# Kernel tuning notes

Hardware: AMD Instinct MI355X
Metric: run time of the kernel (lower is better)

## Reference

```python
import jax, jax.numpy as jnp
import numpy as np

EPS = 1e-12
B, S, H, NH = 4, 2048, 512, 8
DH = H // NH

def layernorm(x, g, b):
    mu = jnp.mean(x, axis=-1, keepdims=True)
    var = jnp.mean((x - mu) ** 2, axis=-1, keepdims=True)
    return (x - mu) * jax.lax.rsqrt(var + EPS) * g + b

def setup_inputs() -> dict:
    key = jax.random.key(0)
    ks = jax.random.split(key, 12)
    s = 0.02
    return {
        "hidden_states": jax.random.normal(ks[0], (B, S, H), dtype=jnp.float32),
        "attention_mask": jnp.zeros((B, 1, 1, S), dtype=jnp.float32),
        "ln1_g": jnp.ones((H,), jnp.float32), "ln1_b": jnp.zeros((H,), jnp.float32),
        "wq": jax.random.normal(ks[1], (H, H), jnp.float32) * s, "bq": jnp.zeros((H,), jnp.float32),
        "wk": jax.random.normal(ks[2], (H, H), jnp.float32) * s, "bk": jnp.zeros((H,), jnp.float32),
        "wv": jax.random.normal(ks[3], (H, H), jnp.float32) * s, "bv": jnp.zeros((H,), jnp.float32),
        "wo": jax.random.normal(ks[4], (H, H), jnp.float32) * s, "bo": jnp.zeros((H,), jnp.float32),
        "ln2_g": jnp.ones((H,), jnp.float32), "ln2_b": jnp.zeros((H,), jnp.float32),
    }

def _heads(x):  # [B,S,H] -> [B,NH,S,DH]
    return x.reshape(B, S, NH, DH).transpose(0, 2, 1, 3)

def reference(hidden_states, attention_mask, ln1_g, ln1_b, wq, bq, wk, bk, wv, bv, wo, bo, ln2_g, ln2_b):
    h = layernorm(hidden_states, ln1_g, ln1_b)  # Pre-LN
    q = _heads(h @ wq.T + bq)
    k = _heads(h @ wk.T + bk)
    v = _heads(h @ wv.T + bv)
    scores = jnp.einsum("bhqd,bhkd->bhqk", q, k) / jnp.sqrt(jnp.float32(DH))
    scores = scores + attention_mask  # additive BERT mask
    probs = jax.nn.softmax(scores, axis=-1)
    ctx = jnp.einsum("bhqk,bhkd->bhqd", probs, v)
    ctx = ctx.transpose(0, 2, 1, 3).reshape(B, S, H)
    # BertSelfOutput: LN(dense(ctx) + residual), residual is the LN'd hidden per module code
    out = layernorm(ctx @ wo.T + bo + h, ln2_g, ln2_b)
    return out
```

## Files before the change

### kernel.cpp

```cpp
#include <hip/hip_runtime.h>

typedef __bf16 bf16;
typedef __bf16 bf16x2 __attribute__((ext_vector_type(2)));
typedef __bf16 bf16x4 __attribute__((ext_vector_type(4)));
typedef __bf16 bf16x8 __attribute__((ext_vector_type(8)));
typedef float f32x4 __attribute__((ext_vector_type(4)));

typedef __attribute__((address_space(1))) const void g_void;
typedef __attribute__((address_space(3))) void l_void;

constexpr int Bsz = 4, S = 2048, H = 512, NH = 8, DH = 64;
constexpr int M = Bsz * S;
constexpr int K = H;
constexpr int WELEM = H * H;
constexpr float LOG2E  = 1.44269504f;
constexpr float QSCALE = 0.125f * LOG2E;

__global__ __launch_bounds__(256) void convert_w(
    const float* __restrict__ w0, const float* __restrict__ w1,
    const float* __restrict__ w2, const float* __restrict__ w3,
    bf16* __restrict__ dst) {
    int y = blockIdx.y;
    const float* src = (y == 0) ? w0 : (y == 1) ? w1 : (y == 2) ? w2 : w3;
    bf16* d = dst + (size_t)y * WELEM;
    int i = (blockIdx.x * 256 + threadIdx.x) * 4;
    float4 v = *(const float4*)(src + i);
    bf16x4 o;
    o.x = (bf16)v.x; o.y = (bf16)v.y; o.z = (bf16)v.z; o.w = (bf16)v.w;
    *(bf16x4*)(d + i) = o;
}

__global__ __launch_bounds__(256) void scale_mask(
    const float* __restrict__ m, float* __restrict__ out) {
    int i = blockIdx.x * 256 + threadIdx.x;
    out[i] = m[i] * LOG2E;
}

__global__ __launch_bounds__(256) void ln_f32_bf16(
    const float* __restrict__ x, const float* __restrict__ g,
    const float* __restrict__ b, bf16* __restrict__ y) {
    int row = blockIdx.x;
    int t = threadIdx.x;
    float2 xv = *(const float2*)(x + (size_t)row * H + t * 2);
    float v0 = xv.x, v1 = xv.y;
    float s = v0 + v1, s2 = v0 * v0 + v1 * v1;
    for (int off = 1; off < 64; off <<= 1) {
        s  += __shfl_xor(s,  off, 64);
        s2 += __shfl_xor(s2, off, 64);
    }
    __shared__ float red[8];
    int wid = t >> 6;
    if ((t & 63) == 0) { red[wid * 2] = s; red[wid * 2 + 1] = s2; }
    __syncthreads();
    s  = red[0] + red[2] + red[4] + red[6];
    s2 = red[1] + red[3] + red[5] + red[7];
    float mu  = s * (1.0f / H);
    float var = s2 * (1.0f / H) - mu * mu;
    float inv = rsqrtf(var + 1e-12f);
    float2 gv = *(const float2*)(g + t * 2);
    float2 bv = *(const float2*)(b + t * 2);
    bf16x2 out;
    out.x = (bf16)((v0 - mu) * inv * gv.x + bv.x);
    out.y = (bf16)((v1 - mu) * inv * gv.y + bv.y);
    *(bf16x2*)(y + (size_t)row * H + t * 2) = out;
}

__global__ __launch_bounds__(256) void ln_bf16_f32(
    const bf16* __restrict__ x, const float* __restrict__ g,
    const float* __restrict__ b, float* __restrict__ y) {
    int row = blockIdx.x;
    int t = threadIdx.x;
    bf16x2 xv = *(const bf16x2*)(x + (size_t)row * H + t * 2);
    float v0 = (float)xv.x, v1 = (float)xv.y;
    float s = v0 + v1, s2 = v0 * v0 + v1 * v1;
    for (int off = 1; off < 64; off <<= 1) {
        s  += __shfl_xor(s,  off, 64);
        s2 += __shfl_xor(s2, off, 64);
    }
    __shared__ float red[8];
    int wid = t >> 6;
    if ((t & 63) == 0) { red[wid * 2] = s; red[wid * 2 + 1] = s2; }
    __syncthreads();
    s  = red[0] + red[2] + red[4] + red[6];
    s2 = red[1] + red[3] + red[5] + red[7];
    float mu  = s * (1.0f / H);
    float var = s2 * (1.0f / H) - mu * mu;
    float inv = rsqrtf(var + 1e-12f);
    float2 gv = *(const float2*)(g + t * 2);
    float2 bv = *(const float2*)(b + t * 2);
    float2 out;
    out.x = (v0 - mu) * inv * gv.x + bv.x;
    out.y = (v1 - mu) * inv * gv.y + bv.y;
    *(float2*)(y + (size_t)row * H + t * 2) = out;
}

__device__ inline void gemm128_mainloop(const bf16* __restrict__ A,
                                        const bf16* __restrict__ W,
                                        int bm, int bn,
                                        bf16* As, bf16* Bs, f32x4 acc[4][4]) {
    int t = threadIdx.x;
    int lane = t & 63, wid = t >> 6;
    int quad = lane >> 4, n = lane & 15;
    int wm = wid & 1, wn = wid >> 1;
    int sw = (n & 7) * 8;
    int srow = lane >> 3;
    int scol = (lane & 7) * 8;
    for (int kt = 0; kt < K; kt += 64) {
        __syncthreads();
        #pragma unroll
        for (int i = 0; i < 4; i++) {
            int chunk = wid * 4 + i;
            int row = chunk * 8 + srow;
            int csrc = scol ^ ((row & 7) * 8);
            __builtin_amdgcn_global_load_lds(
                (g_void*)&A[(size_t)(bm + row) * K + kt + csrc],
                (l_void*)&As[chunk * 512], 16, 0, 0);
            __builtin_amdgcn_global_load_lds(
                (g_void*)&W[(size_t)(bn + row) * K + kt + csrc],
                (l_void*)&Bs[chunk * 512], 16, 0, 0);
        }
        __syncthreads();
        #pragma unroll
        for (int half = 0; half < 2; half++) {
            bf16x8 af[4], bf[4];
            #pragma unroll
            for (int mi = 0; mi < 4; mi++) {
                int c = (half * 32 + quad * 8) ^ sw;
                af[mi] = *(const bf16x8*)&As[(wm * 64 + mi * 16 + n) * 64 + c];
                bf[mi] = *(const bf16x8*)&Bs[(wn * 64 + mi * 16 + n) * 64 + c];
            }
            #pragma unroll
            for (int mi = 0; mi < 4; mi++)
                #pragma unroll
                for (int ni = 0; ni < 4; ni++)
                    acc[mi][ni] = __builtin_amdgcn_mfma_f32_16x16x32_bf16(
                        af[mi], bf[ni], acc[mi][ni], 0, 0, 0);
        }
    }
}

__global__ __launch_bounds__(256) void gemm_qkv(
    const bf16* __restrict__ h, const bf16* __restrict__ wb,
    const float* __restrict__ bq, const float* __restrict__ bk,
    const float* __restrict__ bv,
    bf16* __restrict__ qd, bf16* __restrict__ kd, bf16* __restrict__ vtd) {
    __shared__ alignas(16) bf16 As[128 * 64];
    __shared__ alignas(16) bf16 Bs[128 * 64];
    int bm = blockIdx.x * 128, bn = blockIdx.y * 128, z = blockIdx.z;
    const bf16* W = wb + (size_t)z * WELEM;
    const float* bias = (z == 0) ? bq : (z == 1) ? bk : bv;
    f32x4 acc[4][4];
    for (int mi = 0; mi < 4; mi++)
        for (int ni = 0; ni < 4; ni++)
            for (int r = 0; r < 4; r++) acc[mi][ni][r] = 0.0f;
    gemm128_mainloop(h, W, bm, bn, As, Bs, acc);
    int lane = threadIdx.x & 63, wid = threadIdx.x >> 6;
    int quad = lane >> 4, n = lane & 15;
    int wm = wid & 1, wn = wid >> 1;
    for (int mi = 0; mi < 4; mi++)
        for (int ni = 0; ni < 4; ni++)
            for (int r = 0; r < 4; r++) {
                int i = bm + wm * 64 + mi * 16 + quad * 4 + r;
                int j = bn + wn * 64 + ni * 16 + n;
                float val = acc[mi][ni][r] + bias[j];
                if (z == 0) val *= QSCALE;
                int b = i >> 11, srow = i & (S - 1);
                int nh = j >> 6, d = j & (DH - 1);
                if (z < 2) {
                    bf16* dst = (z == 0) ? qd : kd;
                    dst[(((size_t)(b * NH + nh)) * S + srow) * DH + d] = (bf16)val;
                } else {
                    vtd[(((size_t)(b * NH + nh)) * DH + d) * S + srow] = (bf16)val;
                }
            }
}

__global__ __launch_bounds__(256) void gemm_out(
    const bf16* __restrict__ ctx, const bf16* __restrict__ wo,
    const float* __restrict__ bo, const bf16* __restrict__ resid,
    bf16* __restrict__ dst) {
    __shared__ alignas(16) bf16 As[128 * 64];
    __shared__ alignas(16) bf16 Bs[128 * 64];
    int bm = blockIdx.x * 128, bn = blockIdx.y * 128;
    f32x4 acc[4][4];
    for (int mi = 0; mi < 4; mi++)
        for (int ni = 0; ni < 4; ni++)
            for (int r = 0; r < 4; r++) acc[mi][ni][r] = 0.0f;
    gemm128_mainloop(ctx, wo, bm, bn, As, Bs, acc);
    int lane = threadIdx.x & 63, wid = threadIdx.x >> 6;
    int quad = lane >> 4, n = lane & 15;
    int wm = wid & 1, wn = wid >> 1;
    for (int mi = 0; mi < 4; mi++)
        for (int ni = 0; ni < 4; ni++)
            for (int r = 0; r < 4; r++) {
                int i = bm + wm * 64 + mi * 16 + quad * 4 + r;
                int j = bn + wn * 64 + ni * 16 + n;
                float val = acc[mi][ni][r] + bo[j]
                          + (float)resid[(size_t)i * H + j];
                dst[(size_t)i * H + j] = (bf16)val;
            }
}

constexpr int LDP  = 136;

#if __has_builtin(__builtin_amdgcn_exp2f)
#define EXP2(x) __builtin_amdgcn_exp2f(x)
#else
#define EXP2(x) exp2f(x)
#endif

__global__ __launch_bounds__(512, 4) void attn_kernel(
    const bf16* __restrict__ q, const bf16* __restrict__ k,
    const bf16* __restrict__ vt, const float* __restrict__ mask2,
    bf16* __restrict__ ctx) {
    int bh = blockIdx.y;
    int b = bh >> 3, nh = bh & 7;
    int t = threadIdx.x, wid = t >> 6, lane = t & 63;
    int quad = lane >> 4, n = lane & 15;
    int qbase = blockIdx.x * 128 + wid * 16;

    const bf16* Qp = q  + (size_t)bh * S * DH;
    const bf16* Kp = k  + (size_t)bh * S * DH;
    const bf16* Vt = vt + (size_t)bh * DH * S;
    const float* mrow = mask2 + (size_t)b * S;

    __shared__ alignas(16) bf16 Ks[128 * 64];
    __shared__ alignas(16) bf16 Vs[64 * 128];
    __shared__ alignas(16) bf16 Ps[8][16 * LDP];
    bf16* Pw = Ps[wid];

    int sw = (n & 7) * 8;

    bf16x8 qf[2];
    #pragma unroll
    for (int hh = 0; hh < 2; hh++)
        qf[hh] = *(const bf16x8*)
            &Qp[(size_t)(qbase + n) * DH + hh * 32 + quad * 8];

    f32x4 O[4];
    #pragma unroll
    for (int i = 0; i < 4; i++)
        for (int r = 0; r < 4; r++) O[i][r] = 0.0f;
    float l_run = 0.0f;

    for (int kb = 0; kb < S; kb += 128) {
        __syncthreads();
        #pragma unroll
        for (int i = 0; i < 2; i++) {
            int c = t + i * 512;
            {
                int row = c >> 3, part = c & 7;
                int csrc = (part * 8) ^ ((row & 7) * 8);
                __builtin_amdgcn_global_load_lds(
                    (g_void*)&Kp[(size_t)(kb + row) * DH + csrc],
                    (l_void*)&Ks[c * 8], 16, 0, 0);
            }
            {
                int row = c >> 4, part = c & 15;
                int csrc = (part * 8) ^ ((row & 7) * 8);
                __builtin_amdgcn_global_load_lds(
                    (g_void*)&Vt[(size_t)row * S + kb + csrc],
                    (l_void*)&Vs[c * 8], 16, 0, 0);
            }
        }
        __syncthreads();

        #pragma unroll
        for (int kt = 0; kt < 8; kt++) {
            const bf16* kr = &Ks[(kt * 16 + n) * 64];
            bf16x8 ka = *(const bf16x8*)&kr[(quad * 8) ^ sw];
            bf16x8 kc = *(const bf16x8*)&kr[(32 + quad * 8) ^ sw];
            float4 mk = *(const float4*)&mrow[kb + kt * 16 + quad * 4];
            f32x4 s;
            for (int r = 0; r < 4; r++) s[r] = 0.0f;
            s = __builtin_amdgcn_mfma_f32_16x16x32_bf16(ka, qf[0], s, 0, 0, 0);
            s = __builtin_amdgcn_mfma_f32_16x16x32_bf16(kc, qf[1], s, 0, 0, 0);
            float p0 = EXP2(s[0] + mk.x);
            float p1 = EXP2(s[1] + mk.y);
            float p2 = EXP2(s[2] + mk.z);
            float p3 = EXP2(s[3] + mk.w);
            l_run += (p0 + p1) + (p2 + p3);
            bf16x4 w;
            w[0] = (bf16)p0; w[1] = (bf16)p1; w[2] = (bf16)p2; w[3] = (bf16)p3;
            *(bf16x4*)&Pw[n * LDP + kt * 16 + quad * 4] = w;
        }

        __builtin_amdgcn_s_setprio(1);
        #pragma unroll
        for (int ks = 0; ks < 4; ks++) {
            bf16x8 pf = *(const bf16x8*)&Pw[n * LDP + ks * 32 + quad * 8];
            #pragma unroll
            for (int dt = 0; dt < 4; dt++) {
                bf16x8 vf = *(const bf16x8*)
                    &Vs[(dt * 16 + n) * 128 + ((ks * 32 + quad * 8) ^ sw)];
                O[dt] = __builtin_amdgcn_mfma_f32_16x16x32_bf16(
                    vf, pf, O[dt], 0, 0, 0);
            }
        }
        __builtin_amdgcn_s_setprio(0);
    }

    float l = l_run;
    l += __shfl_xor(l, 16, 64);
    l += __shfl_xor(l, 32, 64);
    float linv = 1.0f / l;
    int srow = qbase + n;
    #pragma unroll
    for (int dt = 0; dt < 4; dt++) {
        bf16x4 o4;
        for (int r = 0; r < 4; r++) o4[r] = (bf16)(O[dt][r] * linv);
        int col = nh * 64 + dt * 16 + quad * 4;
        *(bf16x4*)&ctx[((size_t)(b * S + srow)) * H + col] = o4;
    }
}

extern "C" void kernel_launch(void* const* d_in, const int* in_sizes, int n_in,
                              void* d_out, int out_size, void* d_ws, size_t ws_size,
                              hipStream_t stream) {
    const float* hidden = (const float*)d_in[0];
    const float* mask   = (const float*)d_in[1];
    const float* ln1_g  = (const float*)d_in[2];
    const float* ln1_b  = (const float*)d_in[3];
    const float* wq = (const float*)d_in[4],  *bq = (const float*)d_in[5];
    const float* wk = (const float*)d_in[6],  *bk = (const float*)d_in[7];
    const float* wv = (const float*)d_in[8],  *bv = (const float*)d_in[9];
    const float* wo = (const float*)d_in[10], *bo = (const float*)d_in[11];
    const float* ln2_g = (const float*)d_in[12];
    const float* ln2_b = (const float*)d_in[13];

    const size_t T = (size_t)M * H;
    bf16* wb  = (bf16*)d_ws;
    bf16* h   = wb  + (size_t)4 * WELEM;
    bf16* qd  = h   + T;
    bf16* kd  = qd  + T;
    bf16* vtd = kd  + T;
    bf16* ctx = vtd + T;
    float* mask2 = (float*)(ctx + T);
    bf16* tmp = qd;

    convert_w<<<dim3(WELEM / 1024, 4), 256, 0, stream>>>(wq, wk, wv, wo, wb);
    scale_mask<<<Bsz * S / 256, 256, 0, stream>>>(mask, mask2);
    ln_f32_bf16<<<M, 256, 0, stream>>>(hidden, ln1_g, ln1_b, h);
    gemm_qkv<<<dim3(M / 128, H / 128, 3), 256, 0, stream>>>(
        h, wb, bq, bk, bv, qd, kd, vtd);
    attn_kernel<<<dim3(S / 128, Bsz * NH), 512, 0, stream>>>(qd, kd, vtd, mask2, ctx);
    gemm_out<<<dim3(M / 128, H / 128), 256, 0, stream>>>(
        ctx, wb + (size_t)3 * WELEM, bo, h, tmp);
    ln_bf16_f32<<<M, 256, 0, stream>>>(tmp, ln2_g, ln2_b, (float*)d_out);
}
```

Measured before the change: 205.6 us.

## Split attention key blocks across wave pairs, each wave handling 32 query rows

Each wave now computes 32 query rows (two 16-row tiles) over half of each 128-key block, so every K and V fragment read from LDS feeds two MFMA tiles. Two waves share a query group and merge their partial O and row sums through shared memory at the end, adding one reduction pass and an extra barrier. The aim is to cut LDS read traffic per MFMA. In exchange, per-wave register use grows (two sets of O accumulators and Q fragments).

```diff
diff --git a/kernel.cpp b/kernel.cpp
--- a/kernel.cpp
+++ b/kernel.cpp
@@ -201,7 +201,7 @@
             }
 }
 
-constexpr int LDP  = 136;
+constexpr int LDP9 = 72;
 
 #if __has_builtin(__builtin_amdgcn_exp2f)
 #define EXP2(x) __builtin_amdgcn_exp2f(x)
@@ -217,31 +217,36 @@
     int b = bh >> 3, nh = bh & 7;
     int t = threadIdx.x, wid = t >> 6, lane = t & 63;
     int quad = lane >> 4, n = lane & 15;
-    int qbase = blockIdx.x * 128 + wid * 16;
+    int qg = wid >> 1, kh = wid & 1;
+    int qbase = blockIdx.x * 128 + qg * 32;
+    int kO = kh * 64;
 
     const bf16* Qp = q  + (size_t)bh * S * DH;
     const bf16* Kp = k  + (size_t)bh * S * DH;
     const bf16* Vt = vt + (size_t)bh * DH * S;
     const float* mrow = mask2 + (size_t)b * S;
 
-    __shared__ alignas(16) bf16 Ks[128 * 64];
-    __shared__ alignas(16) bf16 Vs[64 * 128];
-    __shared__ alignas(16) bf16 Ps[8][16 * LDP];
-    bf16* Pw = Ps[wid];
+    __shared__ alignas(16) bf16 smem[34816];
+    bf16* Ks = smem;
+    bf16* Vs = smem + 8192;
+    bf16* Pw = smem + 16384 + wid * (32 * LDP9);
 
     int sw = (n & 7) * 8;
 
-    bf16x8 qf[2];
+    bf16x8 qf[2][2];
     #pragma unroll
-    for (int hh = 0; hh < 2; hh++)
-        qf[hh] = *(const bf16x8*)
-            &Qp[(size_t)(qbase + n) * DH + hh * 32 + quad * 8];
-
-    f32x4 O[4];
+    for (int qt = 0; qt < 2; qt++)
+        #pragma unroll
+        for (int hh = 0; hh < 2; hh++)
+            qf[qt][hh] = *(const bf16x8*)
+                &Qp[(size_t)(qbase + qt * 16 + n) * DH + hh * 32 + quad * 8];
+
+    f32x4 O[2][4];
     #pragma unroll
-    for (int i = 0; i < 4; i++)
-        for (int r = 0; r < 4; r++) O[i][r] = 0.0f;
-    float l_run = 0.0f;
+    for (int qt = 0; qt < 2; qt++)
+        for (int i = 0; i < 4; i++)
+            for (int r = 0; r < 4; r++) O[qt][i][r] = 0.0f;
+    float l_run[2] = {0.0f, 0.0f};
 
     for (int kb = 0; kb < S; kb += 128) {
         __syncthreads();
@@ -266,51 +271,79 @@
         __syncthreads();
 
         #pragma unroll
-        for (int kt = 0; kt < 8; kt++) {
-            const bf16* kr = &Ks[(kt * 16 + n) * 64];
+        for (int kt = 0; kt < 4; kt++) {
+            const bf16* kr = &Ks[(kO + kt * 16 + n) * 64];
             bf16x8 ka = *(const bf16x8*)&kr[(quad * 8) ^ sw];
             bf16x8 kc = *(const bf16x8*)&kr[(32 + quad * 8) ^ sw];
-            float4 mk = *(const float4*)&mrow[kb + kt * 16 + quad * 4];
-            f32x4 s;
-            for (int r = 0; r < 4; r++) s[r] = 0.0f;
-            s = __builtin_amdgcn_mfma_f32_16x16x32_bf16(ka, qf[0], s, 0, 0, 0);
-            s = __builtin_amdgcn_mfma_f32_16x16x32_bf16(kc, qf[1], s, 0, 0, 0);
-            float p0 = EXP2(s[0] + mk.x);
-            float p1 = EXP2(s[1] + mk.y);
-            float p2 = EXP2(s[2] + mk.z);
-            float p3 = EXP2(s[3] + mk.w);
-            l_run += (p0 + p1) + (p2 + p3);
-            bf16x4 w;
-            w[0] = (bf16)p0; w[1] = (bf16)p1; w[2] = (bf16)p2; w[3] = (bf16)p3;
-            *(bf16x4*)&Pw[n * LDP + kt * 16 + quad * 4] = w;
+            float4 mk = *(const float4*)&mrow[kb + kO + kt * 16 + quad * 4];
+            #pragma unroll
+            for (int qt = 0; qt < 2; qt++) {
+                f32x4 s;
+                for (int r = 0; r < 4; r++) s[r] = 0.0f;
+                s = __builtin_amdgcn_mfma_f32_16x16x32_bf16(ka, qf[qt][0], s, 0, 0, 0);
+                s = __builtin_amdgcn_mfma_f32_16x16x32_bf16(kc, qf[qt][1], s, 0, 0, 0);
+                float p0 = EXP2(s[0] + mk.x);
+                float p1 = EXP2(s[1] + mk.y);
+                float p2 = EXP2(s[2] + mk.z);
+                float p3 = EXP2(s[3] + mk.w);
+                l_run[qt] += (p0 + p1) + (p2 + p3);
+                bf16x4 w;
+                w[0] = (bf16)p0; w[1] = (bf16)p1; w[2] = (bf16)p2; w[3] = (bf16)p3;
+                *(bf16x4*)&Pw[(qt * 16 + n) * LDP9 + kt * 16 + quad * 4] = w;
+            }
         }
 
         __builtin_amdgcn_s_setprio(1);
         #pragma unroll
-        for (int ks = 0; ks < 4; ks++) {
-            bf16x8 pf = *(const bf16x8*)&Pw[n * LDP + ks * 32 + quad * 8];
+        for (int ks = 0; ks < 2; ks++)
+            #pragma unroll
+            for (int qt = 0; qt < 2; qt++) {
+                bf16x8 pf = *(const bf16x8*)
+                    &Pw[(qt * 16 + n) * LDP9 + ks * 32 + quad * 8];
+                #pragma unroll
+                for (int dt = 0; dt < 4; dt++) {
+                    bf16x8 vf = *(const bf16x8*)
+                        &Vs[(dt * 16 + n) * 128 + ((kO + ks * 32 + quad * 8) ^ sw)];
+                    O[qt][dt] = __builtin_amdgcn_mfma_f32_16x16x32_bf16(
+                        vf, pf, O[qt][dt], 0, 0, 0);
+                }
+            }
+        __builtin_amdgcn_s_setprio(0);
+    }
+
+    float* Ob = (float*)smem;
+    float* Lb = Ob + 4 * 32 * 68;
+    __syncthreads();
+    if (kh) {
+        #pragma unroll
+        for (int qt = 0; qt < 2; qt++) {
+            #pragma unroll
+            for (int dt = 0; dt < 4; dt++)
+                *(f32x4*)&Ob[(qg * 32 + qt * 16 + n) * 68 + dt * 16 + quad * 4]
+                    = O[qt][dt];
+            Lb[(qg * 2 + qt) * 64 + lane] = l_run[qt];
+        }
+    }
+    __syncthreads();
+    if (!kh) {
+        #pragma unroll
+        for (int qt = 0; qt < 2; qt++) {
+            float l = l_run[qt] + Lb[(qg * 2 + qt) * 64 + lane];
+            l += __shfl_xor(l, 16, 64);
+            l += __shfl_xor(l, 32, 64);
+            float linv = 1.0f / l;
+            int srow = qbase + qt * 16 + n;
             #pragma unroll
             for (int dt = 0; dt < 4; dt++) {
-                bf16x8 vf = *(const bf16x8*)
-                    &Vs[(dt * 16 + n) * 128 + ((ks * 32 + quad * 8) ^ sw)];
-                O[dt] = __builtin_amdgcn_mfma_f32_16x16x32_bf16(
-                    vf, pf, O[dt], 0, 0, 0);
-            }
-        }
-        __builtin_amdgcn_s_setprio(0);
-    }
-
-    float l = l_run;
-    l += __shfl_xor(l, 16, 64);
-    l += __shfl_xor(l, 32, 64);
-    float linv = 1.0f / l;
-    int srow = qbase + n;
-    #pragma unroll
-    for (int dt = 0; dt < 4; dt++) {
-        bf16x4 o4;
-        for (int r = 0; r < 4; r++) o4[r] = (bf16)(O[dt][r] * linv);
-        int col = nh * 64 + dt * 16 + quad * 4;
-        *(bf16x4*)&ctx[((size_t)(b * S + srow)) * H + col] = o4;
+                f32x4 po = *(const f32x4*)
+                    &Ob[(qg * 32 + qt * 16 + n) * 68 + dt * 16 + quad * 4];
+                bf16x4 o4;
+                for (int r = 0; r < 4; r++)
+                    o4[r] = (bf16)((O[qt][dt][r] + po[r]) * linv);
+                int col = nh * 64 + dt * 16 + quad * 4;
+                *(bf16x4*)&ctx[((size_t)(b * S + srow)) * H + col] = o4;
+            }
+        }
     }
 }
 
```

New measurement: 202.1 us. Within noise of the previous version (-1.7%).
